# Kernel optimization log

Hardware: AMD Instinct MI355X
Metric: run time of the kernel (lower is better)

## Reference

```python
import jax, jax.numpy as jnp
import numpy as np

B, N, D = 512, 100000, 64
TAU = 1e-4            # gumbel-softmax temperature from source
SIM_RATIO = 0.5       # similarity_ratio init kwarg
COS_EPS = 1e-6


def setup_inputs() -> dict:
    key = jax.random.key(0)
    k1, k2, k3, k4, k5 = jax.random.split(key, 5)
    need_replace = jax.random.randint(k1, (B, 2), 0, N, dtype=jnp.int64) if jax.config.jax_enable_x64 else jax.random.randint(k1, (B, 2), 0, N, dtype=jnp.int32)
    union_feature = jax.random.normal(k2, (B, 2 * D), dtype=jnp.float32)
    all_items = jax.random.normal(k3, (N, D), dtype=jnp.float32) * 0.1
    W = jax.random.normal(k4, (D, 2 * D), dtype=jnp.float32) * 0.05
    b = jax.random.normal(k5, (D,), dtype=jnp.float32) * 0.01
    return {"need_replace": need_replace, "union_feature": union_feature,
            "all_items": all_items, "W": W, "b": b}


def _cosine(a, b):
    # torch.nn.CosineSimilarity(dim=1, eps=1e-6): dot / max(||a||*||b||, eps)
    dot = jnp.sum(a * b, axis=1)
    na = jnp.linalg.norm(a, axis=1)
    nb = jnp.linalg.norm(b, axis=1)
    return dot / jnp.maximum(na * nb, COS_EPS)


def reference(need_replace, union_feature, all_items, W, b):
    item_ids = need_replace[:, 1]
    items_emb = all_items[item_ids]                      # [B, D]
    uif = union_feature @ W.T + b                        # [B, D] (nn.Linear)
    score = uif @ all_items.T                            # [B, N]

    # gumbel_softmax(tau=1e-4, hard=True), training branch
    g = jax.random.gumbel(jax.random.key(42), score.shape, dtype=score.dtype)
    y_soft = jax.nn.softmax((score + g) / TAU, axis=-1)  # [B, N]
    idx = jnp.argmax(y_soft, axis=-1)                    # [B]
    y_hard = jax.nn.one_hot(idx, N, dtype=score.dtype)
    P = y_hard + y_soft - jax.lax.stop_gradient(y_soft)  # straight-through hard one-hot

    item_sequence = jnp.arange(N, dtype=score.dtype)[None, :]
    replaceable_items = jnp.sum(P * item_sequence, axis=-1).astype(jnp.int32)
    replaceable_feat = P @ all_items                     # [B, D]

    sim = _cosine(items_emb, replaceable_feat)
    sim = (sim + 1.0) / 2.0                              # regularize_similarity
    labels = jnp.full((B,), SIM_RATIO, dtype=sim.dtype)
    similarity_loss = jnp.mean((sim - labels) ** 2)      # SimilarityMarginLoss (assumed MSE-to-margin)
    return replaceable_items, replaceable_feat, similarity_loss, jnp.mean(sim)
```

## Files before the change

### kernel.cpp

```cpp
#include <hip/hip_runtime.h>
#include <cstdint>

#define NITEMS   100000
#define BROWS    512
#define DDIM     64
#define S_BLOCKS 391
#define IPB      256
#define OUT_FEAT 512
#define OUT_LOSS (512 + 512 * 64)
#define OUT_MSIM (OUT_LOSS + 1)

#define BITS_RAW_T 4284334592u
#define G_TE       6.001f

typedef __attribute__((ext_vector_type(8)))  short  bf16x8;
typedef __attribute__((ext_vector_type(16))) float  f32x16;
typedef unsigned long long u64;
typedef uint32_t u32;

#define ROTL(x, r) __builtin_amdgcn_alignbit((x), (x), 32u - (r))

__device__ __forceinline__ u32 threefry_0_42_xor(u32 e) {
    const u32 K1 = 42u;
    const u32 K2 = 0x1BD11BDAu ^ 42u;
    u32 x0 = 0u;
    u32 x1 = e + K1;
#define TFR(r) { x0 += x1; x1 = ROTL(x1, r) ^ x0; }
    TFR(13u) TFR(15u) TFR(26u) TFR(6u)
    x0 += K1;  x1 += K2 + 1u;
    TFR(17u) TFR(29u) TFR(16u) TFR(24u)
    x0 += K2;  x1 += 2u;
    TFR(13u) TFR(15u) TFR(26u) TFR(6u)
    x1 += K1 + 3u;
    TFR(17u) TFR(29u) TFR(16u) TFR(24u)
    x0 += K1;  x1 += K2 + 4u;
    TFR(13u) TFR(15u) TFR(26u) TFR(6u)
    x0 += K2;  x1 += 5u;
#undef TFR
    return x0 ^ x1;
}

__device__ __forceinline__ void threefry_pair(u32 ea, u32 eb, u32& oa, u32& ob) {
    const u32 K1 = 42u;
    const u32 K2 = 0x1BD11BDAu ^ 42u;
    u32 a0 = 0u, a1 = ea + K1;
    u32 b0 = 0u, b1 = eb + K1;
#define TFR2(r) { a0 += a1; b0 += b1; a1 = ROTL(a1, r) ^ a0; b1 = ROTL(b1, r) ^ b0; }
    TFR2(13u) TFR2(15u) TFR2(26u) TFR2(6u)
    a0 += K1; a1 += K2 + 1u;  b0 += K1; b1 += K2 + 1u;
    TFR2(17u) TFR2(29u) TFR2(16u) TFR2(24u)
    a0 += K2; a1 += 2u;       b0 += K2; b1 += 2u;
    TFR2(13u) TFR2(15u) TFR2(26u) TFR2(6u)
    a1 += K1 + 3u;            b1 += K1 + 3u;
    TFR2(17u) TFR2(29u) TFR2(16u) TFR2(24u)
    a0 += K1; a1 += K2 + 4u;  b0 += K1; b1 += K2 + 4u;
    TFR2(13u) TFR2(15u) TFR2(26u) TFR2(6u)
    a0 += K2; a1 += 5u;       b0 += K2; b1 += 5u;
#undef TFR2
    oa = a0 ^ a1; ob = b0 ^ b1;
}

__device__ __forceinline__ float gumbel_from_bits(u32 b) {
    float f = __uint_as_float((b >> 9) | 0x3F800000u) - 1.0f;
    f = fmaxf(f, 1.17549435e-38f);
    return -logf(-logf(f));
}
__device__ __forceinline__ u32 order_map(float v) {
    u32 x = __float_as_uint(v);
    return (x & 0x80000000u) ? ~x : (x | 0x80000000u);
}
__device__ __forceinline__ float unpack_val(u64 p) {
    u32 x = (u32)(p >> 32);
    u32 f = (x & 0x80000000u) ? (x & 0x7FFFFFFFu) : ~x;
    return __uint_as_float(f);
}
__device__ __forceinline__ short f32_to_bf16_rne(float f) {
    u32 b = __float_as_uint(f);
    u32 r = (b + 0x7FFFu + ((b >> 16) & 1u)) >> 16;
    return (short)r;
}
__device__ __forceinline__ float bf16_to_f32(short h) {
    return __uint_as_float(((u32)(uint16_t)h) << 16);
}

__global__ void prep_kernel(const float* __restrict__ UF, const float* __restrict__ W,
                            const float* __restrict__ bias, const float* __restrict__ A,
                            float* __restrict__ uif, float* __restrict__ unorm,
                            float* __restrict__ wsAM4, float* __restrict__ out) {
    const int t = threadIdx.x, b = blockIdx.x;
    if (b == 0 && t == 0) { out[OUT_LOSS] = 0.f; out[OUT_MSIM] = 0.f; }
    if (b < 128) {
        __shared__ float Wt[128 * 65];
        for (int i = t; i < 8192; i += 256) {
            int d = i >> 7, k = i & 127;
            Wt[k * 65 + d] = W[i];
        }
        __syncthreads();
        const int row = b * 4 + (t >> 6);
        const int d   = t & 63;
        const float* u = UF + row * 128;
        float s = 0.f;
#pragma unroll 4
        for (int k = 0; k < 128; k++) s = fmaf(u[k], Wt[k * 65 + d], s);
        s += bias[d];
        uif[row * 64 + d] = s;
        float q = s * s;
#pragma unroll
        for (int o = 32; o >= 1; o >>= 1) q += __shfl_xor(q, o);
        if (d == 0) unorm[row] = sqrtf(q);
    } else {
        const int item = (b - 128) * 256 + t;
        float q = 0.f;
        if (item < NITEMS) {
            const float4* r = (const float4*)(A + (size_t)item * DDIM);
#pragma unroll
            for (int k = 0; k < 16; k++) {
                float4 x = r[k];
                q = fmaf(x.x, x.x, q); q = fmaf(x.y, x.y, q);
                q = fmaf(x.z, x.z, q); q = fmaf(x.w, x.w, q);
            }
        }
        float n = sqrtf(q);
#pragma unroll
        for (int o = 32; o >= 1; o >>= 1) n = fmaxf(n, __shfl_xor(n, o));
        if ((t & 63) == 0) wsAM4[(b - 128) * 4 + (t >> 6)] = n;
    }
}

__global__ __launch_bounds__(256, 4) void phase1_kernel(
        const float* __restrict__ A, const float* __restrict__ uif,
        u64* __restrict__ wsT1, float* __restrict__ wsB) {
    __shared__ bf16x8 sh_ah[4 * 256];
    __shared__ bf16x8 sh_al[4 * 256];
    const int tid  = threadIdx.x;
    const int lane = tid & 63;
    const int wv   = tid >> 6;
    const int rg   = blockIdx.y;
    const int sb   = blockIdx.x;
    const int itembase = sb * IPB;
    const int ntiles = min(8, (NITEMS - itembase + 31) >> 5);
    const int row   = rg * 128 + wv * 32 + (lane & 31);
    const int khalf = (lane >> 5) * 8;

    bf16x8 uh[4], ul[4];
#pragma unroll
    for (int s = 0; s < 4; s++) {
        const float* src = uif + row * 64 + khalf + 16 * s;
        float4 v0 = *(const float4*)src;
        float4 v1 = *(const float4*)(src + 4);
        float vv[8] = {v0.x, v0.y, v0.z, v0.w, v1.x, v1.y, v1.z, v1.w};
        bf16x8 h, l2;
#pragma unroll
        for (int j = 0; j < 8; j++) {
            short hh = f32_to_bf16_rne(vv[j]);
            float r  = vv[j] - bf16_to_f32(hh);
            h[j] = hh; l2[j] = f32_to_bf16_rne(r);
        }
        uh[s] = h; ul[s] = l2;
    }

    u64 t1p = 0ull; float t1f = -3.0e38f, t2f = -3.0e38f, sm = -3.0e38f;
    const u32 rowbase_e = (u32)row * (u32)NITEMS;

    const int s_i   = tid & 31;
    const int s_c   = tid >> 5;
    const int s_dst = (s_c >> 1) * 64 + s_i + 32 * (s_c & 1);
    const float* s_srcbase = A + (size_t)s_i * 64 + 8 * s_c;

    float4 q0[4], q1[4];
#pragma unroll
    for (int j = 0; j < 4; j++) {
        const float* src = s_srcbase + (size_t)(itembase + 32 * j) * 64;
        q0[j] = *(const float4*)(src);
        q1[j] = *(const float4*)(src + 4);
    }

    for (int g = 0; g < 2; g++) {
        const int tbase = g * 4;
        __syncthreads();
#pragma unroll
        for (int j = 0; j < 4; j++) {
            if (tbase + j < ntiles) {
                float vv[8] = {q0[j].x, q0[j].y, q0[j].z, q0[j].w,
                               q1[j].x, q1[j].y, q1[j].z, q1[j].w};
                bf16x8 h, l2;
#pragma unroll
                for (int k = 0; k < 8; k++) {
                    short hh = f32_to_bf16_rne(vv[k]);
                    float r  = vv[k] - bf16_to_f32(hh);
                    h[k] = hh; l2[k] = f32_to_bf16_rne(r);
                }
                sh_ah[j * 256 + s_dst] = h; sh_al[j * 256 + s_dst] = l2;
            }
        }
        __syncthreads();
        if (g == 0) {
#pragma unroll
            for (int j = 0; j < 4; j++) {
                if (4 + j < ntiles) {
                    const float* src = s_srcbase + (size_t)(itembase + 32 * (4 + j)) * 64;
                    q0[j] = *(const float4*)(src);
                    q1[j] = *(const float4*)(src + 4);
                }
            }
        }
#pragma unroll
        for (int j = 0; j < 4; j++) {
            if (tbase + j < ntiles) {
                f32x16 acc;
#pragma unroll
                for (int z = 0; z < 16; z++) acc[z] = 0.0f;
#pragma unroll
                for (int s = 0; s < 4; s++) {
                    bf16x8 ah = sh_ah[j * 256 + s * 64 + lane];
                    bf16x8 al = sh_al[j * 256 + s * 64 + lane];
                    acc = __builtin_amdgcn_mfma_f32_32x32x16_bf16(ah, uh[s], acc, 0, 0, 0);
                    acc = __builtin_amdgcn_mfma_f32_32x32x16_bf16(al, uh[s], acc, 0, 0, 0);
                    acc = __builtin_amdgcn_mfma_f32_32x32x16_bf16(ah, ul[s], acc, 0, 0, 0);
                }
                const int tb  = itembase + (tbase + j) * 32;
                const int ib4 = tb + 4 * (lane >> 5);
#pragma unroll
                for (int i = 0; i < 16; i += 2) {
                    const int il0 = (i & 3) + 8 * (i >> 2);
                    const int il1 = ((i + 1) & 3) + 8 * ((i + 1) >> 2);
                    const int item0 = ib4 + il0;
                    const int item1 = ib4 + il1;
                    u32 r0, r1;
                    threefry_pair(rowbase_e + (u32)item0, rowbase_e + (u32)item1, r0, r1);
                    float sA = acc[i], sB = acc[i + 1];
                    sm = fmaxf(sm, fmaxf(sA, sB));
                    if (r0 >= BITS_RAW_T) {
                        float v = sA + gumbel_from_bits(r0);
                        if (v > t1f) {
                            t2f = t1f; t1f = v;
                            t1p = ((u64)order_map(v) << 32) | (u32)(~(u32)item0);
                        } else t2f = fmaxf(t2f, v);
                    }
                    if (r1 >= BITS_RAW_T) {
                        float v = sB + gumbel_from_bits(r1);
                        if (v > t1f) {
                            t2f = t1f; t1f = v;
                            t1p = ((u64)order_map(v) << 32) | (u32)(~(u32)item1);
                        } else t2f = fmaxf(t2f, v);
                    }
                }
            }
        }
    }

    float bnd = fmaxf(t2f, sm + G_TE);
    {
        u64   op = __shfl_xor(t1p, 32);
        float of = __shfl_xor(t1f, 32);
        float ob = __shfl_xor(bnd, 32);
        if (op > t1p) { bnd = fmaxf(fmaxf(bnd, ob), t1f); t1p = op; t1f = of; }
        else          { bnd = fmaxf(fmaxf(bnd, ob), of); }
    }
    if (lane < 32) {
        wsT1[(size_t)row * S_BLOCKS + sb] = t1p;
        wsB [(size_t)row * S_BLOCKS + sb] = bnd;
    }
}

__global__ __launch_bounds__(256) void rowresolve_kernel(
        const u64* __restrict__ wsT1, const float* __restrict__ wsB,
        const float* __restrict__ wsAM4, const float* __restrict__ unorm,
        const float* __restrict__ uif, const float* __restrict__ A,
        const int* __restrict__ need_replace, float* __restrict__ out) {
    const int row = blockIdx.x, t = threadIdx.x;
    __shared__ float Us[64];
    __shared__ u64   shP[4];
    __shared__ float shF2[4], shAM[4];
    if (t < 64) Us[t] = uif[row * 64 + t];

    float am = 0.f;
    for (int i = t; i < S_BLOCKS * 4; i += 256) am = fmaxf(am, wsAM4[i]);
    u64 p1 = 0ull; float f1 = -3.0e38f, f2 = -3.0e38f;
    for (int sbk = t; sbk < S_BLOCKS; sbk += 256) {
        u64   ep = wsT1[(size_t)row * S_BLOCKS + sbk];
        float e2 = wsB [(size_t)row * S_BLOCKS + sbk];
        if (ep > p1) { f2 = fmaxf(fmaxf(f1, e2), f2); p1 = ep; f1 = unpack_val(ep); }
        else         { float v = unpack_val(ep); f2 = fmaxf(f2, fmaxf(v, e2)); }
    }
#pragma unroll
    for (int off = 1; off < 64; off <<= 1) {
        u64   op  = __shfl_xor(p1, off);
        float of1 = __shfl_xor(f1, off);
        float of2 = __shfl_xor(f2, off);
        am = fmaxf(am, __shfl_xor(am, off));
        if (op > p1) { f2 = fmaxf(fmaxf(f1, of2), f2); p1 = op; f1 = of1; }
        else         { f2 = fmaxf(f2, fmaxf(of1, of2)); }
    }
    if ((t & 63) == 0) { shP[t >> 6] = p1; shF2[t >> 6] = f2; shAM[t >> 6] = am; }
    __syncthreads();

    u64 P = shP[0]; float F1 = unpack_val(P), F2 = shF2[0], AM = shAM[0];
#pragma unroll
    for (int w = 1; w < 4; w++) {
        u64 op = shP[w]; float o2 = shF2[w];
        AM = fmaxf(AM, shAM[w]);
        if (op > P) { F2 = fmaxf(fmaxf(F1, o2), F2); P = op; F1 = unpack_val(op); }
        else        { F2 = fmaxf(F2, fmaxf(unpack_val(op), o2)); }
    }
    const float E = 1.5e-4f * unorm[row] * AM + 3.0e-5f;

    if (!(F1 - F2 > 2.0f * E)) {
        const float thresh = F1 - 2.0f * E;
        u64 pk = 0ull;
        for (int sb = 0; sb < S_BLOCKS; sb++) {
            u64   tp = wsT1[(size_t)row * S_BLOCKS + sb];
            float bb = wsB [(size_t)row * S_BLOCKS + sb];
            if (fmaxf(unpack_val(tp), bb) >= thresh) {
                const int item = sb * IPB + t;
                if (item < NITEMS) {
                    u32 rb  = threefry_0_42_xor((u32)row * (u32)NITEMS + (u32)item);
                    float g = gumbel_from_bits(rb);
                    const float4* a4 = (const float4*)(A + (size_t)item * DDIM);
                    float s0 = 0.f, s1 = 0.f;
#pragma unroll
                    for (int k = 0; k < 16; k += 2) {
                        float4 x = a4[k];
                        float4 y = a4[k + 1];
                        s0 = fmaf(x.x, Us[4*k    ], s0);
                        s0 = fmaf(x.y, Us[4*k + 1], s0);
                        s0 = fmaf(x.z, Us[4*k + 2], s0);
                        s0 = fmaf(x.w, Us[4*k + 3], s0);
                        s1 = fmaf(y.x, Us[4*k + 4], s1);
                        s1 = fmaf(y.y, Us[4*k + 5], s1);
                        s1 = fmaf(y.z, Us[4*k + 6], s1);
                        s1 = fmaf(y.w, Us[4*k + 7], s1);
                    }
                    float v = (s0 + s1) + g;
                    u64 c = ((u64)order_map(v) << 32) | (u32)(~(u32)item);
                    if (c > pk) pk = c;
                }
            }
        }
#pragma unroll
        for (int off = 1; off < 64; off <<= 1) {
            u64 o = __shfl_xor(pk, off);
            pk = (o > pk) ? o : pk;
        }
        __syncthreads();
        if ((t & 63) == 0) shP[t >> 6] = pk;
        __syncthreads();
        P = shP[0];
#pragma unroll
        for (int w = 1; w < 4; w++) if (shP[w] > P) P = shP[w];
    }

    if (t < 64) {
        const int idx = (int)(~(u32)(P & 0xFFFFFFFFull));
        float fr = A[(size_t)idx * DDIM + t];
        out[OUT_FEAT + row * DDIM + t] = fr;
        int   item = need_replace[2 * row + 1];
        float fa   = A[(size_t)item * DDIM + t];
        float dot = fa * fr, na2 = fa * fa, nb2 = fr * fr;
#pragma unroll
        for (int o = 32; o >= 1; o >>= 1) {
            dot += __shfl_down(dot, o);
            na2 += __shfl_down(na2, o);
            nb2 += __shfl_down(nb2, o);
        }
        if (t == 0) {
            out[row] = (float)idx;
            float denom = fmaxf(sqrtf(na2) * sqrtf(nb2), 1e-6f);
            float sim = (dot / denom + 1.0f) * 0.5f;
            float d = sim - 0.5f;
            atomicAdd(&out[OUT_LOSS], d * d * (1.0f / 512.0f));
            atomicAdd(&out[OUT_MSIM], sim * (1.0f / 512.0f));
        }
    }
}

extern "C" void kernel_launch(void* const* d_in, const int* in_sizes, int n_in,
                              void* d_out, int out_size, void* d_ws, size_t ws_size,
                              hipStream_t stream) {
    (void)in_sizes; (void)n_in; (void)out_size; (void)ws_size;
    const int*   need_replace = (const int*)d_in[0];
    const float* UF           = (const float*)d_in[1];
    const float* A            = (const float*)d_in[2];
    const float* W            = (const float*)d_in[3];
    const float* bias         = (const float*)d_in[4];
    float* out = (float*)d_out;

    char* ws = (char*)d_ws;
    u64*   wsT1    = (u64*)  (ws);
    float* wsB     = (float*)(ws + 1601536);
    float* uif     = (float*)(ws + 2402304);
    float* unorm   = (float*)(ws + 2533376);
    float* wsAM4   = (float*)(ws + 2535424);

    prep_kernel<<<519, 256, 0, stream>>>(UF, W, bias, A, uif, unorm, wsAM4, out);
    phase1_kernel<<<dim3(S_BLOCKS, 4), 256, 0, stream>>>(A, uif, wsT1, wsB);
    rowresolve_kernel<<<BROWS, 256, 0, stream>>>(wsT1, wsB, wsAM4, unorm, uif, A,
                                                 need_replace, out);
}
```

Measured before the change: 258.0 us.

## Fuse three kernels into one cooperative kernel with grid syncs

Merges the prep, phase1 and rowresolve kernels into a single persistent cooperative kernel of 1024 blocks. The stages are separated by grid.sync, and phase1 work units are looped over with a grid stride. This is meant to remove two kernel launch boundaries and their gaps. In exchange it adds grid-wide barriers, reduces phase1 parallelism to one wave of 1024 blocks covering 1564 units, and shares 33 KB of static LDS across all stages, which may limit occupancy. A fallback to the three separate launches is kept in case the cooperative launch fails.

```diff
diff --git a/kernel.cpp b/kernel.cpp
--- a/kernel.cpp
+++ b/kernel.cpp
@@ -1,11 +1,16 @@
 #include <hip/hip_runtime.h>
+#include <hip/hip_cooperative_groups.h>
 #include <cstdint>
+
+namespace cg = cooperative_groups;
 
 #define NITEMS   100000
 #define BROWS    512
 #define DDIM     64
 #define S_BLOCKS 391
 #define IPB      256
+#define NUNITS   1564
+#define COOP_GRID 1024
 #define OUT_FEAT 512
 #define OUT_LOSS (512 + 512 * 64)
 #define OUT_MSIM (OUT_LOSS + 1)
@@ -83,14 +88,15 @@
     return __uint_as_float(((u32)(uint16_t)h) << 16);
 }
 
-__global__ void prep_kernel(const float* __restrict__ UF, const float* __restrict__ W,
-                            const float* __restrict__ bias, const float* __restrict__ A,
-                            float* __restrict__ uif, float* __restrict__ unorm,
-                            float* __restrict__ wsAM4, float* __restrict__ out) {
-    const int t = threadIdx.x, b = blockIdx.x;
+
+__device__ __forceinline__ void prep_body(int b, int t,
+        const float* __restrict__ UF, const float* __restrict__ W,
+        const float* __restrict__ bias, const float* __restrict__ A,
+        float* __restrict__ uif, float* __restrict__ unorm,
+        float* __restrict__ wsAM4, float* __restrict__ out, char* smem) {
     if (b == 0 && t == 0) { out[OUT_LOSS] = 0.f; out[OUT_MSIM] = 0.f; }
     if (b < 128) {
-        __shared__ float Wt[128 * 65];
+        float* Wt = (float*)smem;
         for (int i = t; i < 8192; i += 256) {
             int d = i >> 7, k = i & 127;
             Wt[k * 65 + d] = W[i];
@@ -127,16 +133,13 @@
     }
 }
 
-__global__ __launch_bounds__(256, 4) void phase1_kernel(
+__device__ __forceinline__ void phase1_body(int sb, int rg, int tid,
         const float* __restrict__ A, const float* __restrict__ uif,
-        u64* __restrict__ wsT1, float* __restrict__ wsB) {
-    __shared__ bf16x8 sh_ah[4 * 256];
-    __shared__ bf16x8 sh_al[4 * 256];
-    const int tid  = threadIdx.x;
+        u64* __restrict__ wsT1, float* __restrict__ wsB, char* smem) {
+    bf16x8* sh_ah = (bf16x8*)smem;
+    bf16x8* sh_al = (bf16x8*)(smem + 16384);
     const int lane = tid & 63;
     const int wv   = tid >> 6;
-    const int rg   = blockIdx.y;
-    const int sb   = blockIdx.x;
     const int itembase = sb * IPB;
     const int ntiles = min(8, (NITEMS - itembase + 31) >> 5);
     const int row   = rg * 128 + wv * 32 + (lane & 31);
@@ -263,15 +266,15 @@
     }
 }
 
-__global__ __launch_bounds__(256) void rowresolve_kernel(
+__device__ __forceinline__ void rowresolve_body(int row, int t,
         const u64* __restrict__ wsT1, const float* __restrict__ wsB,
         const float* __restrict__ wsAM4, const float* __restrict__ unorm,
         const float* __restrict__ uif, const float* __restrict__ A,
-        const int* __restrict__ need_replace, float* __restrict__ out) {
-    const int row = blockIdx.x, t = threadIdx.x;
-    __shared__ float Us[64];
-    __shared__ u64   shP[4];
-    __shared__ float shF2[4], shAM[4];
+        const int* __restrict__ need_replace, float* __restrict__ out, char* smem) {
+    float* Us   = (float*)smem;
+    u64*   shP  = (u64*)(smem + 256);
+    float* shF2 = (float*)(smem + 288);
+    float* shAM = (float*)(smem + 304);
     if (t < 64) Us[t] = uif[row * 64 + t];
 
     float am = 0.f;
@@ -374,6 +377,55 @@
     }
 }
 
+__global__ __launch_bounds__(256, 4) void fused_all(
+        const float* __restrict__ UF, const float* __restrict__ W,
+        const float* __restrict__ bias, const float* __restrict__ A,
+        const int* __restrict__ need_replace,
+        float* __restrict__ uif, float* __restrict__ unorm,
+        float* __restrict__ wsAM4, u64* __restrict__ wsT1, float* __restrict__ wsB,
+        float* __restrict__ out) {
+    __shared__ __align__(16) char smem[33280];
+    cg::grid_group grid = cg::this_grid();
+    const int bx = blockIdx.x, t = threadIdx.x;
+
+    if (bx < 519) prep_body(bx, t, UF, W, bias, A, uif, unorm, wsAM4, out, smem);
+    __threadfence();
+    grid.sync();
+
+    for (int u = bx; u < NUNITS; u += COOP_GRID)
+        phase1_body(u % S_BLOCKS, u / S_BLOCKS, t, A, uif, wsT1, wsB, smem);
+    __threadfence();
+    grid.sync();
+
+    if (bx < BROWS)
+        rowresolve_body(bx, t, wsT1, wsB, wsAM4, unorm, uif, A, need_replace, out, smem);
+}
+
+__global__ void prep_kernel(const float* __restrict__ UF, const float* __restrict__ W,
+                            const float* __restrict__ bias, const float* __restrict__ A,
+                            float* __restrict__ uif, float* __restrict__ unorm,
+                            float* __restrict__ wsAM4, float* __restrict__ out) {
+    __shared__ __align__(16) char smem[33280];
+    prep_body(blockIdx.x, threadIdx.x, UF, W, bias, A, uif, unorm, wsAM4, out, smem);
+}
+
+__global__ __launch_bounds__(256, 4) void phase1_kernel(
+        const float* __restrict__ A, const float* __restrict__ uif,
+        u64* __restrict__ wsT1, float* __restrict__ wsB) {
+    __shared__ __align__(16) char smem[32768];
+    phase1_body(blockIdx.x, blockIdx.y, threadIdx.x, A, uif, wsT1, wsB, smem);
+}
+
+__global__ __launch_bounds__(256) void rowresolve_kernel(
+        const u64* __restrict__ wsT1, const float* __restrict__ wsB,
+        const float* __restrict__ wsAM4, const float* __restrict__ unorm,
+        const float* __restrict__ uif, const float* __restrict__ A,
+        const int* __restrict__ need_replace, float* __restrict__ out) {
+    __shared__ __align__(16) char smem[512];
+    rowresolve_body(blockIdx.x, threadIdx.x, wsT1, wsB, wsAM4, unorm, uif, A,
+                    need_replace, out, smem);
+}
+
 extern "C" void kernel_launch(void* const* d_in, const int* in_sizes, int n_in,
                               void* d_out, int out_size, void* d_ws, size_t ws_size,
                               hipStream_t stream) {
@@ -392,8 +444,15 @@
     float* unorm   = (float*)(ws + 2533376);
     float* wsAM4   = (float*)(ws + 2535424);
 
-    prep_kernel<<<519, 256, 0, stream>>>(UF, W, bias, A, uif, unorm, wsAM4, out);
-    phase1_kernel<<<dim3(S_BLOCKS, 4), 256, 0, stream>>>(A, uif, wsT1, wsB);
-    rowresolve_kernel<<<BROWS, 256, 0, stream>>>(wsT1, wsB, wsAM4, unorm, uif, A,
-                                                 need_replace, out);
-}
+    void* args[] = { (void*)&UF, (void*)&W, (void*)&bias, (void*)&A,
+                     (void*)&need_replace, (void*)&uif, (void*)&unorm,
+                     (void*)&wsAM4, (void*)&wsT1, (void*)&wsB, (void*)&out };
+    hipError_t err = hipLaunchCooperativeKernel((void*)fused_all, dim3(COOP_GRID),
+                                                dim3(256), args, 0, stream);
+    if (err != hipSuccess) {
+        prep_kernel<<<519, 256, 0, stream>>>(UF, W, bias, A, uif, unorm, wsAM4, out);
+        phase1_kernel<<<dim3(S_BLOCKS, 4), 256, 0, stream>>>(A, uif, wsT1, wsB);
+        rowresolve_kernel<<<BROWS, 256, 0, stream>>>(wsT1, wsB, wsAM4, unorm, uif, A,
+                                                     need_replace, out);
+    }
+}
```

After: 670.9 us. 160% more time.
